# Optimization experiments

Hardware: AMD Instinct MI355X
Metric: run time of the kernel (lower is better)

## Reference

```python
import jax, jax.numpy as jnp
import numpy as np

N, C, H, W = 2, 256, 64, 64   # feature map
K = 64                        # number of boxes
PH = PW = 7                   # output_size
SCALE = 0.25                  # spatial_scale
SR = 2                        # sampling_ratio


def setup_inputs() -> dict:
    key = jax.random.key(0)
    k1, k2, k3, k4 = jax.random.split(key, 4)
    features = jax.random.normal(k1, (N, C, H, W), dtype=jnp.float32)
    masks = jax.random.uniform(k2, (K, C, H, W), dtype=jnp.float32)
    bidx = jax.random.randint(k3, (K,), 0, N).astype(jnp.float32)
    # box corners in image coordinates [0, W/SCALE)
    pts = jax.random.uniform(k4, (K, 4), minval=0.0, maxval=W / SCALE, dtype=jnp.float32)
    x1 = jnp.minimum(pts[:, 0], pts[:, 2]); x2 = jnp.maximum(pts[:, 0], pts[:, 2])
    y1 = jnp.minimum(pts[:, 1], pts[:, 3]); y2 = jnp.maximum(pts[:, 1], pts[:, 3])
    boxes = jnp.stack([bidx, x1, y1, x2, y2], axis=1)  # [K, 5]
    return {"features": features, "boxes": boxes, "masks": masks}


def _bilinear(fmap, ys, xs):
    """Bilinear sample fmap[C,H,W] at all (ys x xs) grid points -> [C, Ny, Nx].
    Matches torchvision RoIAlign edge handling (zero outside [-1, L])."""
    Hh, Ww = fmap.shape[1], fmap.shape[2]

    def ax(v, L):
        valid = (v >= -1.0) & (v <= L)
        vc = jnp.clip(v, 0.0, L - 1.0)
        lo = jnp.floor(vc).astype(jnp.int32)
        hi = jnp.minimum(lo + 1, L - 1)
        fr = vc - lo.astype(vc.dtype)
        return valid, lo, hi, fr

    vy, yl, yh, ly = ax(ys, Hh)
    vx, xl, xh, lx = ax(xs, Ww)
    hy, hx = 1.0 - ly, 1.0 - lx
    g = lambda yi, xi: fmap[:, yi[:, None], xi[None, :]]  # [C, Ny, Nx]
    val = (hy[:, None] * hx[None, :]) * g(yl, xl) \
        + (hy[:, None] * lx[None, :]) * g(yl, xh) \
        + (ly[:, None] * hx[None, :]) * g(yh, xl) \
        + (ly[:, None] * lx[None, :]) * g(yh, xh)
    return val * (vy[:, None] & vx[None, :]).astype(val.dtype)


def reference(features, boxes, masks):
    b = boxes[:, 0].astype(jnp.int32)                      # batch index per box
    coords = jax.lax.stop_gradient(boxes[:, 1:]) * SCALE   # roi_align has no box grad
    off = (jnp.arange(SR, dtype=jnp.float32) + 0.5) / SR   # sub-bin offsets

    def one(bi, box, mask):
        fmap = features[bi] * mask                         # masked clone [C,H,W]
        x1, y1, x2, y2 = box
        roi_w = jnp.maximum(x2 - x1, 1.0)
        roi_h = jnp.maximum(y2 - y1, 1.0)
        bin_h, bin_w = roi_h / PH, roi_w / PW
        ys = (y1 + (jnp.arange(PH, dtype=jnp.float32)[:, None] + off) * bin_h).reshape(-1)
        xs = (x1 + (jnp.arange(PW, dtype=jnp.float32)[:, None] + off) * bin_w).reshape(-1)
        vals = _bilinear(fmap, ys, xs)                     # [C, PH*SR, PW*SR]
        return vals.reshape(fmap.shape[0], PH, SR, PW, SR).mean(axis=(2, 4))

    return jax.vmap(one)(b, coords, masks)                 # [K, C, PH, PW]
```

## Files before the change

### kernel.cpp

```cpp
#include <hip/hip_runtime.h>
#include <hip/hip_bf16.h>
#include <hip/hip_fp16.h>


constexpr int N_ = 2, C_ = 256, H_ = 64, W_ = 64;
constexpr int K_ = 64, PH_ = 7, PW_ = 7, SR_ = 2;
constexpr float SCALE_ = 0.25f;
constexpr int CG = 2;
constexpr int BT = 128;

__global__ __launch_bounds__(BT)
void masked_roialign_h16(const float* __restrict__ features,
                         const float* __restrict__ boxes,
                         const float* __restrict__ masks,
                         float* __restrict__ out) {
    __shared__ __half prod[CG][H_ * W_];

    const int k  = blockIdx.x;
    const int cg = blockIdx.y;
    const int t  = threadIdx.x;

    const float* bx = boxes + k * 5;
    const int   b  = (int)bx[0];
    const float x1 = bx[1] * SCALE_;
    const float y1 = bx[2] * SCALE_;
    const float x2 = bx[3] * SCALE_;
    const float y2 = bx[4] * SCALE_;
    const float roi_w = fmaxf(x2 - x1, 1.0f);
    const float roi_h = fmaxf(y2 - y1, 1.0f);
    const float bin_w = roi_w * (1.0f / PW_);
    const float bin_h = roi_h * (1.0f / PH_);

    const float ymin_c = fminf(fmaxf(y1 + 0.25f * bin_h, 0.0f), (float)(H_ - 1));
    const float ymax_c = fminf(fmaxf(y1 + 6.75f * bin_h, 0.0f), (float)(H_ - 1));
    const int ylo   = (int)ymin_c;
    const int yhi   = min((int)ymax_c + 1, H_ - 1);
    const int nrows = yhi - ylo + 1;

    const int tx = (t & 15) << 2;
    const int ty = t >> 4;
#pragma unroll
    for (int cl = 0; cl < CG; ++cl) {
        const int c = cg * CG + cl;
        const float* fb = features + ((size_t)b * C_ + c) * (H_ * W_);
        const float* mb = masks    + ((size_t)k * C_ + c) * (H_ * W_);
        for (int r = ty; r < nrows; r += 8) {
            const int row = ylo + r;
            const float4 fv = *(const float4*)(fb + row * W_ + tx);
            const float4 mv = *(const float4*)(mb + row * W_ + tx);
            __half2* dst = (__half2*)&prod[cl][row * W_ + tx];
            dst[0] = __floats2half2_rn(fv.x * mv.x, fv.y * mv.y);
            dst[1] = __floats2half2_rn(fv.z * mv.z, fv.w * mv.w);
        }
    }
    __syncthreads();

    const int cl  = t >> 6;
    const int bin = t & 63;
    if (bin >= PH_ * PW_) return;
    const int ph = bin / PW_;
    const int pw = bin - ph * PW_;

    const __half* __restrict__ p = prod[cl];

    float acc = 0.0f;
#pragma unroll
    for (int iy = 0; iy < SR_; ++iy) {
        const float y  = y1 + ((float)ph + ((float)iy + 0.5f) * 0.5f) * bin_h;
        const bool  vy = (y >= -1.0f) && (y <= (float)H_);
        const float yc = fminf(fmaxf(y, 0.0f), (float)(H_ - 1));
        const int   yl = (int)yc;
        const int   yh = min(yl + 1, H_ - 1);
        const float ly = yc - (float)yl;
        const float hy = 1.0f - ly;
        const int   rl = yl * W_;
        const int   rh = yh * W_;
#pragma unroll
        for (int ix = 0; ix < SR_; ++ix) {
            const float x  = x1 + ((float)pw + ((float)ix + 0.5f) * 0.5f) * bin_w;
            const bool  vx = (x >= -1.0f) && (x <= (float)W_);
            const float xc = fminf(fmaxf(x, 0.0f), (float)(W_ - 1));
            const int   xl = (int)xc;
            const int   xh = min(xl + 1, W_ - 1);
            const float lx = xc - (float)xl;
            const float hx = 1.0f - lx;

            const float v00 = __half2float(p[rl + xl]);
            const float v01 = __half2float(p[rl + xh]);
            const float v10 = __half2float(p[rh + xl]);
            const float v11 = __half2float(p[rh + xh]);
            const float val = hy * hx * v00 + hy * lx * v01
                            + ly * hx * v10 + ly * lx * v11;
            acc += (vy && vx) ? val : 0.0f;
        }
    }
    const int c = cg * CG + cl;
    out[(((size_t)k * C_ + c) * PH_ + ph) * PW_ + pw] = acc * 0.25f;
}

extern "C" void kernel_launch(void* const* d_in, const int* in_sizes, int n_in,
                              void* d_out, int out_size, void* d_ws, size_t ws_size,
                              hipStream_t stream) {
    const float* features = (const float*)d_in[0];
    const float* boxes    = (const float*)d_in[1];
    const float* masks    = (const float*)d_in[2];
    float* out            = (float*)d_out;

    dim3 grid(K_, C_ / CG);
    dim3 block(BT);
    masked_roialign_h16<<<grid, block, 0, stream>>>(features, boxes, masks, out);
}
```

Before: 338.2 us.

## Load only sampled mask rows, batch channel loads, use nontemporal mask reads

When the ROI spans more rows than there are sample rows, each block now loads only the 28 feature/mask rows that bilinear sampling actually reads, instead of every row in the ROI's vertical range. Channels per block and threads per block are doubled, and all channel loads for a row are issued before the multiplies and shared-memory stores to expose more memory-level parallelism. Mask loads use nontemporal hints because each mask element is read only once. The main goal is to cut global mask traffic, which dominates the kernel. The cost is per-slot row index arithmetic, and fewer blocks in the grid.

```diff
diff --git a/kernel.cpp b/kernel.cpp
--- a/kernel.cpp
+++ b/kernel.cpp
@@ -6,15 +6,18 @@
 constexpr int N_ = 2, C_ = 256, H_ = 64, W_ = 64;
 constexpr int K_ = 64, PH_ = 7, PW_ = 7, SR_ = 2;
 constexpr float SCALE_ = 0.25f;
-constexpr int CG = 2;
-constexpr int BT = 128;
+constexpr int CG = 4;
+constexpr int BT = 256;
+constexpr int HW = H_ * W_;
+
+typedef float vf4 __attribute__((ext_vector_type(4)));
 
 __global__ __launch_bounds__(BT)
-void masked_roialign_h16(const float* __restrict__ features,
-                         const float* __restrict__ boxes,
-                         const float* __restrict__ masks,
-                         float* __restrict__ out) {
-    __shared__ __half prod[CG][H_ * W_];
+void masked_roialign_r5(const float* __restrict__ features,
+                        const float* __restrict__ boxes,
+                        const float* __restrict__ masks,
+                        float* __restrict__ out) {
+    __shared__ __half prod[CG][HW];
 
     const int k  = blockIdx.x;
     const int cg = blockIdx.y;
@@ -37,20 +40,41 @@
     const int yhi   = min((int)ymax_c + 1, H_ - 1);
     const int nrows = yhi - ylo + 1;
 
-    const int tx = (t & 15) << 2;
-    const int ty = t >> 4;
+    {
+        const int tx = (t & 15) << 2;
+        const int ty = t >> 4;
+        const int c0 = cg * CG;
+        const float* fb = features + ((size_t)b * C_ + c0) * HW;
+        const float* mb = masks    + ((size_t)k * C_ + c0) * HW;
+        const bool sparse = (nrows > 2 * PH_ * SR_);
+        const int  nslots = sparse ? 2 * PH_ * SR_ : nrows;
+
+        for (int slot = ty; slot < nslots; slot += 16) {
+            int row;
+            if (sparse) {
+                const int   s  = slot >> 1;
+                const int   ph = s >> 1;
+                const int   iy = s & 1;
+                const float y  = y1 + ((float)ph + ((float)iy + 0.5f) * 0.5f) * bin_h;
+                const float yc = fminf(fmaxf(y, 0.0f), (float)(H_ - 1));
+                const int   yl = (int)yc;
+                row = (slot & 1) ? min(yl + 1, H_ - 1) : yl;
+            } else {
+                row = ylo + slot;
+            }
+            const int off = row * W_ + tx;
+            vf4 fv[CG], mv[CG];
 #pragma unroll
-    for (int cl = 0; cl < CG; ++cl) {
-        const int c = cg * CG + cl;
-        const float* fb = features + ((size_t)b * C_ + c) * (H_ * W_);
-        const float* mb = masks    + ((size_t)k * C_ + c) * (H_ * W_);
-        for (int r = ty; r < nrows; r += 8) {
-            const int row = ylo + r;
-            const float4 fv = *(const float4*)(fb + row * W_ + tx);
-            const float4 mv = *(const float4*)(mb + row * W_ + tx);
-            __half2* dst = (__half2*)&prod[cl][row * W_ + tx];
-            dst[0] = __floats2half2_rn(fv.x * mv.x, fv.y * mv.y);
-            dst[1] = __floats2half2_rn(fv.z * mv.z, fv.w * mv.w);
+            for (int cl = 0; cl < CG; ++cl) {
+                fv[cl] = *(const vf4*)(fb + (size_t)cl * HW + off);
+                mv[cl] = __builtin_nontemporal_load((const vf4*)(mb + (size_t)cl * HW + off));
+            }
+#pragma unroll
+            for (int cl = 0; cl < CG; ++cl) {
+                __half2* d = (__half2*)&prod[cl][off];
+                d[0] = __floats2half2_rn(fv[cl].x * mv[cl].x, fv[cl].y * mv[cl].y);
+                d[1] = __floats2half2_rn(fv[cl].z * mv[cl].z, fv[cl].w * mv[cl].w);
+            }
         }
     }
     __syncthreads();
@@ -108,5 +132,5 @@
 
     dim3 grid(K_, C_ / CG);
     dim3 block(BT);
-    masked_roialign_h16<<<grid, block, 0, stream>>>(features, boxes, masks, out);
+    masked_roialign_r5<<<grid, block, 0, stream>>>(features, boxes, masks, out);
 }
```

Result: faster. 320.0 us (-5.4%).
